# Kernel optimization log

Measured on AMD Instinct MI355X. Metric: run time of the kernel, lower is better.

The kernel has to match this reference:

```python
import jax, jax.numpy as jnp
import numpy as np

N = 50000   # nodes
E = 600000  # edges
D = 128     # in = hidden = out channels
L = 3       # num_layers
LN_EPS = 1e-5


def setup_inputs() -> dict:
    key = jax.random.key(0)
    ks = jax.random.split(key, 4)
    x = jax.random.normal(ks[0], (N, D), dtype=jnp.float32)
    edge_index = jax.random.randint(ks[1], (2, E), 0, N, dtype=jnp.int32)
    # GCNConv linear weights (glorot-ish scale) and biases, one per layer
    Ws = jax.random.normal(ks[2], (L, D, D), dtype=jnp.float32) / np.sqrt(D)
    bs = jnp.zeros((L, D), dtype=jnp.float32)
    # LayerNorm affine params per layer
    ln_w = jnp.ones((L, D), dtype=jnp.float32)
    ln_b = jnp.zeros((L, D), dtype=jnp.float32)
    # PReLU (single shared slope per layer, torch default init 0.25)
    alphas = jnp.full((L,), 0.25, dtype=jnp.float32)
    return {"x": x, "edge_index": edge_index, "Ws": Ws, "bs": bs,
            "ln_w": ln_w, "ln_b": ln_b, "alphas": alphas}


def reference(x, edge_index, Ws, bs, ln_w, ln_b, alphas):
    # --- gcn_norm: add self-loops, symmetric D^{-1/2} (A+I) D^{-1/2} ---
    loop = jnp.arange(N, dtype=edge_index.dtype)
    src = jnp.concatenate([edge_index[0], loop])  # [E+N]
    dst = jnp.concatenate([edge_index[1], loop])  # [E+N]
    deg = jax.ops.segment_sum(jnp.ones_like(dst, dtype=x.dtype), dst,
                              num_segments=N)
    dinv = jnp.where(deg > 0, jax.lax.rsqrt(jnp.maximum(deg, 1.0)), 0.0)
    norm = (dinv[src] * dinv[dst])[:, None]  # [E+N, 1]

    h = x
    for l in range(L):
        # GCNConv: linear -> gather -> scale -> scatter-add -> bias
        h = h @ Ws[l]                                   # [N, D]
        msg = h[src] * norm                             # [E+N, D]
        h = jax.ops.segment_sum(msg, dst, num_segments=N) + bs[l]
        # LayerNorm over feature dim
        mu = jnp.mean(h, axis=-1, keepdims=True)
        var = jnp.mean((h - mu) ** 2, axis=-1, keepdims=True)
        h = (h - mu) * jax.lax.rsqrt(var + LN_EPS) * ln_w[l] + ln_b[l]
        # PReLU
        h = jnp.where(h >= 0, h, alphas[l] * h)
    return h
```

## Files before the change

### kernel.cpp

```cpp
#include <hip/hip_runtime.h>
#include <hip/hip_bf16.h>

#define NN 50000
#define EE 600000
#define DD 128
#define LL 3
#define LN_EPS 1e-5f
#define CAP 64
#define ALD 136
#define POOL 16
#define NBLKS (NN / POOL)

typedef __attribute__((ext_vector_type(8))) short short8;
typedef __attribute__((ext_vector_type(4))) float floatx4;

__device__ inline unsigned short f2bf(float f) {
    union { float f; unsigned u; } a; a.f = f;
    unsigned r = a.u + 0x7fffu + ((a.u >> 16) & 1u);
    return (unsigned short)(r >> 16);
}


__global__ __launch_bounds__(256) void init_kernel(const float* __restrict__ W,
                                                   unsigned short* __restrict__ Wt,
                                                   int* __restrict__ cnt) {
    for (int i = blockIdx.x * 256 + threadIdx.x; i < NN; i += gridDim.x * 256)
        cnt[i] = 0;
    for (int i = blockIdx.x * 256 + threadIdx.x; i < LL * DD * DD; i += gridDim.x * 256) {
        int l = i >> 14, n = (i >> 7) & 127, k = i & 127;
        Wt[i] = f2bf(W[(l << 14) + k * DD + n]);
    }
}


__global__ __launch_bounds__(256) void gemm0_fill_kernel(
    const float* __restrict__ A, const unsigned short* __restrict__ Wt,
    const int* __restrict__ src, const int* __restrict__ dst,
    int* __restrict__ cnt, int* __restrict__ csrc,
    unsigned short* __restrict__ Cb) {
    __shared__ unsigned short alds[POOL * ALD];
    int tid = threadIdx.x;
    int lane = tid & 63;
    int w = tid >> 6;

    {
        int e = blockIdx.x * 256 + tid;
        if (e < EE) {
            int d = dst[e];
            int pos = atomicAdd(&cnt[d], 1);
            csrc[(size_t)d * CAP + pos] = src[e];
        }
    }

    {
        int row = tid >> 4;
        int kc = (tid & 15) * 8;
        const float* ap = &A[(size_t)(blockIdx.x * POOL + row) * DD + kc];
        float4 v0 = *(const float4*)&ap[0];
        float4 v1 = *(const float4*)&ap[4];
        float fv[8] = {v0.x, v0.y, v0.z, v0.w, v1.x, v1.y, v1.z, v1.w};
        unsigned short uv[8];
        #pragma unroll
        for (int q = 0; q < 8; q++) uv[q] = f2bf(fv[q]);
        *(uint4*)&alds[row * ALD + kc] = *(uint4*)&uv[0];
    }
    __syncthreads();

    int cbase = w * 32;
    int kq = (lane >> 4) * 8;
    int mrow = lane & 15;
    floatx4 acc[2] = {{0.f,0.f,0.f,0.f},{0.f,0.f,0.f,0.f}};
    #pragma unroll
    for (int t = 0; t < 4; t++) {
        short8 a = *(const short8*)&alds[mrow * ALD + t * 32 + kq];
        #pragma unroll
        for (int j = 0; j < 2; j++) {
            short8 b = *(const short8*)&Wt[(cbase + j * 16 + (lane & 15)) * DD + t * 32 + kq];
            acc[j] = __builtin_amdgcn_mfma_f32_16x16x32_bf16(a, b, acc[j], 0, 0, 0);
        }
    }
    __syncthreads();

    {
        int r0 = (lane >> 4) * 4;
        #pragma unroll
        for (int i = 0; i < 4; i++)
            #pragma unroll
            for (int j = 0; j < 2; j++)
                alds[(r0 + i) * ALD + cbase + j * 16 + (lane & 15)] = f2bf(acc[j][i]);
    }
    __syncthreads();
    {
        int srow = tid >> 4;
        int scol = (tid & 15) * 8;
        *(uint4*)&Cb[(size_t)(blockIdx.x * POOL + srow) * DD + scol] =
            *(uint4*)&alds[srow * ALD + scol];
    }
}


__device__ inline void acc_row_w(float* acc, uint4 t, float w) {
    unsigned uu[4] = {t.x, t.y, t.z, t.w};
    #pragma unroll
    for (int q = 0; q < 4; q++) {
        union { unsigned x; float f; } lo, hi;
        lo.x = uu[q] << 16;
        hi.x = uu[q] & 0xffff0000u;
        acc[2 * q]     += w * lo.f;
        acc[2 * q + 1] += w * hi.f;
    }
}

__device__ inline void agg_node(const unsigned short* __restrict__ Tb,
                                const int* __restrict__ cnt, const int* __restrict__ csrc,
                                const float* bv, const float* wv, const float* cv,
                                float alpha, int node, int f8, float* yv) {
    int deg = cnt[node];
    float dv = rsqrtf((float)(deg + 1));
    const int* row = &csrc[(size_t)node * CAP];

    float acc[8] = {};
    acc_row_w(acc, *(const uint4*)&Tb[(size_t)node * DD + f8], dv);

    int k = 0;
    for (; k + 4 <= deg; k += 4) {
        int4 ss = *(const int4*)&row[k];
        float w0 = rsqrtf((float)(cnt[ss.x] + 1));
        float w1 = rsqrtf((float)(cnt[ss.y] + 1));
        float w2 = rsqrtf((float)(cnt[ss.z] + 1));
        float w3 = rsqrtf((float)(cnt[ss.w] + 1));
        uint4 t0 = *(const uint4*)&Tb[(size_t)ss.x * DD + f8];
        uint4 t1 = *(const uint4*)&Tb[(size_t)ss.y * DD + f8];
        uint4 t2 = *(const uint4*)&Tb[(size_t)ss.z * DD + f8];
        uint4 t3 = *(const uint4*)&Tb[(size_t)ss.w * DD + f8];
        acc_row_w(acc, t0, w0); acc_row_w(acc, t1, w1);
        acc_row_w(acc, t2, w2); acc_row_w(acc, t3, w3);
    }
    for (; k < deg; k++) {
        int s = row[k];
        float w = rsqrtf((float)(cnt[s] + 1));
        acc_row_w(acc, *(const uint4*)&Tb[(size_t)s * DD + f8], w);
    }

    float a[8];
    float s1 = 0.f, s2 = 0.f;
    #pragma unroll
    for (int q = 0; q < 8; q++) {
        a[q] = fmaf(acc[q], dv, bv[q]);
        s1 += a[q]; s2 += a[q] * a[q];
    }
    #pragma unroll
    for (int off = 8; off > 0; off >>= 1) {
        s1 += __shfl_xor(s1, off, 16);
        s2 += __shfl_xor(s2, off, 16);
    }
    float mu = s1 * (1.f / DD);
    float var = s2 * (1.f / DD) - mu * mu;
    float rstd = rsqrtf(var + LN_EPS);
    #pragma unroll
    for (int q = 0; q < 8; q++) {
        float y = (a[q] - mu) * rstd * wv[q] + cv[q];
        yv[q] = (y >= 0.f) ? y : alpha * y;
    }
}


__global__ __launch_bounds__(256) void aggemm_kernel(
    const unsigned short* __restrict__ Tb, const int* __restrict__ cnt,
    const int* __restrict__ csrc,
    const float* __restrict__ bias, const float* __restrict__ lnw,
    const float* __restrict__ lnb, const float* __restrict__ alphas, int layer,
    const unsigned short* __restrict__ Wt, unsigned short* __restrict__ Tout) {
    __shared__ unsigned short alds[POOL * ALD];
    int tid = threadIdx.x;
    int g = tid >> 4;
    int lane16 = tid & 15;
    int f8 = lane16 * 8;
    int nodebase = blockIdx.x * POOL;

    float4 b0 = *(const float4*)&bias[f8];
    float4 b1 = *(const float4*)&bias[f8 + 4];
    float4 w0 = *(const float4*)&lnw[f8];
    float4 w1 = *(const float4*)&lnw[f8 + 4];
    float4 c0 = *(const float4*)&lnb[f8];
    float4 c1 = *(const float4*)&lnb[f8 + 4];
    float bv[8] = {b0.x, b0.y, b0.z, b0.w, b1.x, b1.y, b1.z, b1.w};
    float wv[8] = {w0.x, w0.y, w0.z, w0.w, w1.x, w1.y, w1.z, w1.w};
    float cv[8] = {c0.x, c0.y, c0.z, c0.w, c1.x, c1.y, c1.z, c1.w};
    float alpha = alphas[layer];

    {
        int node = nodebase + g;
        float yv[8];
        agg_node(Tb, cnt, csrc, bv, wv, cv, alpha, node, f8, yv);
        unsigned short pv[8];
        #pragma unroll
        for (int q = 0; q < 8; q++) pv[q] = f2bf(yv[q]);
        *(uint4*)&alds[g * ALD + f8] = *(uint4*)&pv[0];
    }
    __syncthreads();

    int lane = tid & 63;
    int w = tid >> 6;
    int cbase = w * 32;
    int kq = (lane >> 4) * 8;
    int mrow = lane & 15;
    floatx4 acc[2] = {{0.f,0.f,0.f,0.f},{0.f,0.f,0.f,0.f}};
    #pragma unroll
    for (int t = 0; t < 4; t++) {
        short8 a = *(const short8*)&alds[mrow * ALD + t * 32 + kq];
        #pragma unroll
        for (int j = 0; j < 2; j++) {
            short8 b = *(const short8*)&Wt[(cbase + j * 16 + (lane & 15)) * DD + t * 32 + kq];
            acc[j] = __builtin_amdgcn_mfma_f32_16x16x32_bf16(a, b, acc[j], 0, 0, 0);
        }
    }
    __syncthreads();

    {
        int r0 = (lane >> 4) * 4;
        #pragma unroll
        for (int i = 0; i < 4; i++)
            #pragma unroll
            for (int j = 0; j < 2; j++)
                alds[(r0 + i) * ALD + cbase + j * 16 + (lane & 15)] = f2bf(acc[j][i]);
    }
    __syncthreads();
    {
        int srow = tid >> 4;
        int scol = (tid & 15) * 8;
        *(uint4*)&Tout[(size_t)(nodebase + srow) * DD + scol] =
            *(uint4*)&alds[srow * ALD + scol];
    }
}


__global__ __launch_bounds__(256) void agg_final_kernel(
    const unsigned short* __restrict__ Tb, const int* __restrict__ cnt,
    const int* __restrict__ csrc,
    const float* __restrict__ bias, const float* __restrict__ lnw,
    const float* __restrict__ lnb, const float* __restrict__ alphas, int layer,
    float* __restrict__ out) {
    int g = threadIdx.x >> 4;
    int lane16 = threadIdx.x & 15;
    int f8 = lane16 * 8;
    int node = blockIdx.x * 16 + g;

    float4 b0 = *(const float4*)&bias[f8];
    float4 b1 = *(const float4*)&bias[f8 + 4];
    float4 w0 = *(const float4*)&lnw[f8];
    float4 w1 = *(const float4*)&lnw[f8 + 4];
    float4 c0 = *(const float4*)&lnb[f8];
    float4 c1 = *(const float4*)&lnb[f8 + 4];
    float bv[8] = {b0.x, b0.y, b0.z, b0.w, b1.x, b1.y, b1.z, b1.w};
    float wv[8] = {w0.x, w0.y, w0.z, w0.w, w1.x, w1.y, w1.z, w1.w};
    float cv[8] = {c0.x, c0.y, c0.z, c0.w, c1.x, c1.y, c1.z, c1.w};

    float yv[8];
    agg_node(Tb, cnt, csrc, bv, wv, cv, alphas[layer], node, f8, yv);

    float* op = &out[(size_t)node * DD + f8];
    *(float4*)&op[0] = make_float4(yv[0], yv[1], yv[2], yv[3]);
    *(float4*)&op[4] = make_float4(yv[4], yv[5], yv[6], yv[7]);
}


extern "C" void kernel_launch(void* const* d_in, const int* in_sizes, int n_in,
                              void* d_out, int out_size, void* d_ws, size_t ws_size,
                              hipStream_t stream) {
    const float* x    = (const float*)d_in[0];
    const int*   ei   = (const int*)d_in[1];
    const float* Ws   = (const float*)d_in[2];
    const float* bs   = (const float*)d_in[3];
    const float* lnw  = (const float*)d_in[4];
    const float* lnb  = (const float*)d_in[5];
    const float* alphas = (const float*)d_in[6];
    float* out = (float*)d_out;

    const int* src = ei;
    const int* dst = ei + EE;

    char* ws = (char*)d_ws;
    size_t off = 0;
    auto alloc = [&](size_t bytes) -> void* {
        void* p = ws + off;
        off = (off + bytes + 255) & ~(size_t)255;
        return p;
    };
    int* cnt  = (int*)alloc(NN * sizeof(int));
    int* csrc = (int*)alloc((size_t)NN * CAP * sizeof(int));
    unsigned short* wt    = (unsigned short*)alloc((size_t)LL * DD * DD * sizeof(unsigned short));
    unsigned short* tbufA = (unsigned short*)alloc((size_t)NN * DD * sizeof(unsigned short));
    unsigned short* tbufB = (unsigned short*)alloc((size_t)NN * DD * sizeof(unsigned short));

    init_kernel<<<256, 256, 0, stream>>>(Ws, wt, cnt);
    gemm0_fill_kernel<<<NBLKS, 256, 0, stream>>>(x, wt, src, dst, cnt, csrc, tbufA);

    aggemm_kernel<<<NBLKS, 256, 0, stream>>>(tbufA, cnt, csrc,
                                             bs + 0 * DD, lnw + 0 * DD, lnb + 0 * DD,
                                             alphas, 0, wt + 1 * DD * DD, tbufB);
    aggemm_kernel<<<NBLKS, 256, 0, stream>>>(tbufB, cnt, csrc,
                                             bs + 1 * DD, lnw + 1 * DD, lnb + 1 * DD,
                                             alphas, 1, wt + 2 * DD * DD, tbufA);
    agg_final_kernel<<<NBLKS, 256, 0, stream>>>(tbufA, cnt, csrc,
                                                bs + 2 * DD, lnw + 2 * DD, lnb + 2 * DD,
                                                alphas, 2, out);
}
```

Baseline: 233.2 us.

## Use persistent blocks with atomic ticket tile scheduling across all kernels

```diff
diff --git a/kernel.cpp b/kernel.cpp
--- a/kernel.cpp
+++ b/kernel.cpp
@@ -9,7 +9,8 @@
 #define CAP 64
 #define ALD 136
 #define POOL 16
-#define NBLKS (NN / POOL)
+#define NTILES (NN / POOL)
+#define GRID 2048
 
 typedef __attribute__((ext_vector_type(8))) short short8;
 typedef __attribute__((ext_vector_type(4))) float floatx4;
@@ -23,9 +24,11 @@
 
 __global__ __launch_bounds__(256) void init_kernel(const float* __restrict__ W,
                                                    unsigned short* __restrict__ Wt,
-                                                   int* __restrict__ cnt) {
+                                                   int* __restrict__ cnt,
+                                                   int* __restrict__ tk) {
     for (int i = blockIdx.x * 256 + threadIdx.x; i < NN; i += gridDim.x * 256)
         cnt[i] = 0;
+    if (blockIdx.x == 0 && threadIdx.x < 4) tk[threadIdx.x] = 0;
     for (int i = blockIdx.x * 256 + threadIdx.x; i < LL * DD * DD; i += gridDim.x * 256) {
         int l = i >> 14, n = (i >> 7) & 127, k = i & 127;
         Wt[i] = f2bf(W[(l << 14) + k * DD + n]);
@@ -37,64 +40,68 @@
     const float* __restrict__ A, const unsigned short* __restrict__ Wt,
     const int* __restrict__ src, const int* __restrict__ dst,
     int* __restrict__ cnt, int* __restrict__ csrc,
-    unsigned short* __restrict__ Cb) {
+    unsigned short* __restrict__ Cb, int* __restrict__ ticket) {
     __shared__ unsigned short alds[POOL * ALD];
+    __shared__ int s_t;
     int tid = threadIdx.x;
     int lane = tid & 63;
     int w = tid >> 6;
 
-    {
-        int e = blockIdx.x * 256 + tid;
-        if (e < EE) {
-            int d = dst[e];
-            int pos = atomicAdd(&cnt[d], 1);
-            csrc[(size_t)d * CAP + pos] = src[e];
-        }
-    }
-
-    {
-        int row = tid >> 4;
-        int kc = (tid & 15) * 8;
-        const float* ap = &A[(size_t)(blockIdx.x * POOL + row) * DD + kc];
-        float4 v0 = *(const float4*)&ap[0];
-        float4 v1 = *(const float4*)&ap[4];
-        float fv[8] = {v0.x, v0.y, v0.z, v0.w, v1.x, v1.y, v1.z, v1.w};
-        unsigned short uv[8];
-        #pragma unroll
-        for (int q = 0; q < 8; q++) uv[q] = f2bf(fv[q]);
-        *(uint4*)&alds[row * ALD + kc] = *(uint4*)&uv[0];
-    }
-    __syncthreads();
-
+    for (int e = blockIdx.x * 256 + tid; e < EE; e += GRID * 256) {
+        int d = dst[e];
+        int s = src[e];
+        int pos = atomicAdd(&cnt[d], 1);
+        csrc[(size_t)d * CAP + pos] = s;
+    }
+
+    int row = tid >> 4;
+    int kc = (tid & 15) * 8;
     int cbase = w * 32;
     int kq = (lane >> 4) * 8;
     int mrow = lane & 15;
-    floatx4 acc[2] = {{0.f,0.f,0.f,0.f},{0.f,0.f,0.f,0.f}};
-    #pragma unroll
-    for (int t = 0; t < 4; t++) {
-        short8 a = *(const short8*)&alds[mrow * ALD + t * 32 + kq];
+
+    for (;;) {
+        if (tid == 0) s_t = atomicAdd(ticket, 1);
+        __syncthreads();
+        int t = s_t;
+        if (t >= NTILES) break;
+        int nodebase = t * POOL;
+
+        {
+            const float* ap = &A[(size_t)(nodebase + row) * DD + kc];
+            float4 v0 = *(const float4*)&ap[0];
+            float4 v1 = *(const float4*)&ap[4];
+            float fv[8] = {v0.x, v0.y, v0.z, v0.w, v1.x, v1.y, v1.z, v1.w};
+            unsigned short uv[8];
+            #pragma unroll
+            for (int q = 0; q < 8; q++) uv[q] = f2bf(fv[q]);
+            *(uint4*)&alds[row * ALD + kc] = *(uint4*)&uv[0];
+        }
+        __syncthreads();
+
+        floatx4 acc[2] = {{0.f,0.f,0.f,0.f},{0.f,0.f,0.f,0.f}};
         #pragma unroll
-        for (int j = 0; j < 2; j++) {
-            short8 b = *(const short8*)&Wt[(cbase + j * 16 + (lane & 15)) * DD + t * 32 + kq];
-            acc[j] = __builtin_amdgcn_mfma_f32_16x16x32_bf16(a, b, acc[j], 0, 0, 0);
-        }
-    }
-    __syncthreads();
-
-    {
-        int r0 = (lane >> 4) * 4;
-        #pragma unroll
-        for (int i = 0; i < 4; i++)
-            #pragma unroll
-            for (int j = 0; j < 2; j++)
-                alds[(r0 + i) * ALD + cbase + j * 16 + (lane & 15)] = f2bf(acc[j][i]);
-    }
-    __syncthreads();
-    {
-        int srow = tid >> 4;
-        int scol = (tid & 15) * 8;
-        *(uint4*)&Cb[(size_t)(blockIdx.x * POOL + srow) * DD + scol] =
-            *(uint4*)&alds[srow * ALD + scol];
+        for (int t4 = 0; t4 < 4; t4++) {
+            short8 a = *(const short8*)&alds[mrow * ALD + t4 * 32 + kq];
+            #pragma unroll
+            for (int j = 0; j < 2; j++) {
+                short8 b = *(const short8*)&Wt[(cbase + j * 16 + (lane & 15)) * DD + t4 * 32 + kq];
+                acc[j] = __builtin_amdgcn_mfma_f32_16x16x32_bf16(a, b, acc[j], 0, 0, 0);
+            }
+        }
+        __syncthreads();
+
+        {
+            int r0 = (lane >> 4) * 4;
+            #pragma unroll
+            for (int i = 0; i < 4; i++)
+                #pragma unroll
+                for (int j = 0; j < 2; j++)
+                    alds[(r0 + i) * ALD + cbase + j * 16 + (lane & 15)] = f2bf(acc[j][i]);
+        }
+        __syncthreads();
+        *(uint4*)&Cb[(size_t)(nodebase + row) * DD + kc] =
+            *(uint4*)&alds[row * ALD + kc];
     }
 }
 
@@ -170,13 +177,14 @@
     const int* __restrict__ csrc,
     const float* __restrict__ bias, const float* __restrict__ lnw,
     const float* __restrict__ lnb, const float* __restrict__ alphas, int layer,
-    const unsigned short* __restrict__ Wt, unsigned short* __restrict__ Tout) {
+    const unsigned short* __restrict__ Wt, unsigned short* __restrict__ Tout,
+    int* __restrict__ ticket) {
     __shared__ unsigned short alds[POOL * ALD];
+    __shared__ int s_t;
     int tid = threadIdx.x;
     int g = tid >> 4;
     int lane16 = tid & 15;
     int f8 = lane16 * 8;
-    int nodebase = blockIdx.x * POOL;
 
     float4 b0 = *(const float4*)&bias[f8];
     float4 b1 = *(const float4*)&bias[f8 + 4];
@@ -189,48 +197,53 @@
     float cv[8] = {c0.x, c0.y, c0.z, c0.w, c1.x, c1.y, c1.z, c1.w};
     float alpha = alphas[layer];
 
-    {
-        int node = nodebase + g;
-        float yv[8];
-        agg_node(Tb, cnt, csrc, bv, wv, cv, alpha, node, f8, yv);
-        unsigned short pv[8];
-        #pragma unroll
-        for (int q = 0; q < 8; q++) pv[q] = f2bf(yv[q]);
-        *(uint4*)&alds[g * ALD + f8] = *(uint4*)&pv[0];
-    }
-    __syncthreads();
-
     int lane = tid & 63;
     int w = tid >> 6;
     int cbase = w * 32;
     int kq = (lane >> 4) * 8;
     int mrow = lane & 15;
-    floatx4 acc[2] = {{0.f,0.f,0.f,0.f},{0.f,0.f,0.f,0.f}};
-    #pragma unroll
-    for (int t = 0; t < 4; t++) {
-        short8 a = *(const short8*)&alds[mrow * ALD + t * 32 + kq];
+
+    for (;;) {
+        if (tid == 0) s_t = atomicAdd(ticket, 1);
+        __syncthreads();
+        int t = s_t;
+        if (t >= NTILES) break;
+        int nodebase = t * POOL;
+
+        {
+            int node = nodebase + g;
+            float yv[8];
+            agg_node(Tb, cnt, csrc, bv, wv, cv, alpha, node, f8, yv);
+            unsigned short pv[8];
+            #pragma unroll
+            for (int q = 0; q < 8; q++) pv[q] = f2bf(yv[q]);
+            *(uint4*)&alds[g * ALD + f8] = *(uint4*)&pv[0];
+        }
+        __syncthreads();
+
+        floatx4 acc[2] = {{0.f,0.f,0.f,0.f},{0.f,0.f,0.f,0.f}};
         #pragma unroll
-        for (int j = 0; j < 2; j++) {
-            short8 b = *(const short8*)&Wt[(cbase + j * 16 + (lane & 15)) * DD + t * 32 + kq];
-            acc[j] = __builtin_amdgcn_mfma_f32_16x16x32_bf16(a, b, acc[j], 0, 0, 0);
-        }
-    }
-    __syncthreads();
-
-    {
-        int r0 = (lane >> 4) * 4;
-        #pragma unroll
-        for (int i = 0; i < 4; i++)
-            #pragma unroll
-            for (int j = 0; j < 2; j++)
-                alds[(r0 + i) * ALD + cbase + j * 16 + (lane & 15)] = f2bf(acc[j][i]);
-    }
-    __syncthreads();
-    {
-        int srow = tid >> 4;
-        int scol = (tid & 15) * 8;
-        *(uint4*)&Tout[(size_t)(nodebase + srow) * DD + scol] =
-            *(uint4*)&alds[srow * ALD + scol];
+        for (int t4 = 0; t4 < 4; t4++) {
+            short8 a = *(const short8*)&alds[mrow * ALD + t4 * 32 + kq];
+            #pragma unroll
+            for (int j = 0; j < 2; j++) {
+                short8 b = *(const short8*)&Wt[(cbase + j * 16 + (lane & 15)) * DD + t4 * 32 + kq];
+                acc[j] = __builtin_amdgcn_mfma_f32_16x16x32_bf16(a, b, acc[j], 0, 0, 0);
+            }
+        }
+        __syncthreads();
+
+        {
+            int r0 = (lane >> 4) * 4;
+            #pragma unroll
+            for (int i = 0; i < 4; i++)
+                #pragma unroll
+                for (int j = 0; j < 2; j++)
+                    alds[(r0 + i) * ALD + cbase + j * 16 + (lane & 15)] = f2bf(acc[j][i]);
+        }
+        __syncthreads();
+        *(uint4*)&Tout[(size_t)(nodebase + g) * DD + f8] =
+            *(uint4*)&alds[g * ALD + f8];
     }
 }
 
@@ -240,11 +253,12 @@
     const int* __restrict__ csrc,
     const float* __restrict__ bias, const float* __restrict__ lnw,
     const float* __restrict__ lnb, const float* __restrict__ alphas, int layer,
-    float* __restrict__ out) {
-    int g = threadIdx.x >> 4;
-    int lane16 = threadIdx.x & 15;
+    float* __restrict__ out, int* __restrict__ ticket) {
+    __shared__ int s_t;
+    int tid = threadIdx.x;
+    int g = tid >> 4;
+    int lane16 = tid & 15;
     int f8 = lane16 * 8;
-    int node = blockIdx.x * 16 + g;
 
     float4 b0 = *(const float4*)&bias[f8];
     float4 b1 = *(const float4*)&bias[f8 + 4];
@@ -255,13 +269,22 @@
     float bv[8] = {b0.x, b0.y, b0.z, b0.w, b1.x, b1.y, b1.z, b1.w};
     float wv[8] = {w0.x, w0.y, w0.z, w0.w, w1.x, w1.y, w1.z, w1.w};
     float cv[8] = {c0.x, c0.y, c0.z, c0.w, c1.x, c1.y, c1.z, c1.w};
-
-    float yv[8];
-    agg_node(Tb, cnt, csrc, bv, wv, cv, alphas[layer], node, f8, yv);
-
-    float* op = &out[(size_t)node * DD + f8];
-    *(float4*)&op[0] = make_float4(yv[0], yv[1], yv[2], yv[3]);
-    *(float4*)&op[4] = make_float4(yv[4], yv[5], yv[6], yv[7]);
+    float alpha = alphas[layer];
+
+    for (;;) {
+        if (tid == 0) s_t = atomicAdd(ticket, 1);
+        __syncthreads();
+        int t = s_t;
+        if (t >= NTILES) break;
+        int node = t * POOL + g;
+
+        float yv[8];
+        agg_node(Tb, cnt, csrc, bv, wv, cv, alpha, node, f8, yv);
+
+        float* op = &out[(size_t)node * DD + f8];
+        *(float4*)&op[0] = make_float4(yv[0], yv[1], yv[2], yv[3]);
+        *(float4*)&op[4] = make_float4(yv[4], yv[5], yv[6], yv[7]);
+    }
 }
 
 
@@ -292,17 +315,18 @@
     unsigned short* wt    = (unsigned short*)alloc((size_t)LL * DD * DD * sizeof(unsigned short));
     unsigned short* tbufA = (unsigned short*)alloc((size_t)NN * DD * sizeof(unsigned short));
     unsigned short* tbufB = (unsigned short*)alloc((size_t)NN * DD * sizeof(unsigned short));
-
-    init_kernel<<<256, 256, 0, stream>>>(Ws, wt, cnt);
-    gemm0_fill_kernel<<<NBLKS, 256, 0, stream>>>(x, wt, src, dst, cnt, csrc, tbufA);
-
-    aggemm_kernel<<<NBLKS, 256, 0, stream>>>(tbufA, cnt, csrc,
-                                             bs + 0 * DD, lnw + 0 * DD, lnb + 0 * DD,
-                                             alphas, 0, wt + 1 * DD * DD, tbufB);
-    aggemm_kernel<<<NBLKS, 256, 0, stream>>>(tbufB, cnt, csrc,
-                                             bs + 1 * DD, lnw + 1 * DD, lnb + 1 * DD,
-                                             alphas, 1, wt + 2 * DD * DD, tbufA);
-    agg_final_kernel<<<NBLKS, 256, 0, stream>>>(tbufA, cnt, csrc,
-                                                bs + 2 * DD, lnw + 2 * DD, lnb + 2 * DD,
-                                                alphas, 2, out);
-}
+    int* tk = (int*)alloc(4 * sizeof(int));
+
+    init_kernel<<<256, 256, 0, stream>>>(Ws, wt, cnt, tk);
+    gemm0_fill_kernel<<<GRID, 256, 0, stream>>>(x, wt, src, dst, cnt, csrc, tbufA, tk + 0);
+
+    aggemm_kernel<<<GRID, 256, 0, stream>>>(tbufA, cnt, csrc,
+                                            bs + 0 * DD, lnw + 0 * DD, lnb + 0 * DD,
+                                            alphas, 0, wt + 1 * DD * DD, tbufB, tk + 1);
+    aggemm_kernel<<<GRID, 256, 0, stream>>>(tbufB, cnt, csrc,
+                                            bs + 1 * DD, lnw + 1 * DD, lnb + 1 * DD,
+                                            alphas, 1, wt + 2 * DD * DD, tbufA, tk + 2);
+    agg_final_kernel<<<GRID, 256, 0, stream>>>(tbufA, cnt, csrc,
+                                               bs + 2 * DD, lnw + 2 * DD, lnb + 2 * DD,
+                                               alphas, 2, out, tk + 3);
+}
```

Result: slower. 377.3 us (+61.8%).

## Prescale GEMM output by source dinv and split edge fill from first GEMM

Applied to the files above, without the earlier changes.

```diff
diff --git a/kernel.cpp b/kernel.cpp
--- a/kernel.cpp
+++ b/kernel.cpp
@@ -7,12 +7,15 @@
 #define LL 3
 #define LN_EPS 1e-5f
 #define CAP 64
+#define CNTS 16
 #define ALD 136
 #define POOL 16
-#define NBLKS (NN / POOL)
+#define NTILES (NN / POOL)
+#define FILLB ((EE + 255) / 256)
 
 typedef __attribute__((ext_vector_type(8))) short short8;
 typedef __attribute__((ext_vector_type(4))) float floatx4;
+typedef __attribute__((ext_vector_type(4))) unsigned uintx4;
 
 __device__ inline unsigned short f2bf(float f) {
     union { float f; unsigned u; } a; a.f = f;
@@ -20,42 +23,48 @@
     return (unsigned short)(r >> 16);
 }
 
-
-__global__ __launch_bounds__(256) void init_kernel(const float* __restrict__ W,
-                                                   unsigned short* __restrict__ Wt,
-                                                   int* __restrict__ cnt) {
-    for (int i = blockIdx.x * 256 + threadIdx.x; i < NN; i += gridDim.x * 256)
-        cnt[i] = 0;
-    for (int i = blockIdx.x * 256 + threadIdx.x; i < LL * DD * DD; i += gridDim.x * 256) {
+__device__ inline uintx4 gload4(const unsigned short* p) {
+    uintx4 r;
+    asm volatile("global_load_dwordx4 %0, %1, off" : "=v"(r) : "v"(p));
+    return r;
+}
+
+
+__global__ __launch_bounds__(256) void fill_kernel(
+    const float* __restrict__ W, unsigned short* __restrict__ Wt,
+    const int* __restrict__ src, const int* __restrict__ dst,
+    int* __restrict__ cnt, int* __restrict__ csrc) {
+    int e = blockIdx.x * 256 + threadIdx.x;
+    for (int i = e; i < LL * DD * DD; i += FILLB * 256) {
         int l = i >> 14, n = (i >> 7) & 127, k = i & 127;
         Wt[i] = f2bf(W[(l << 14) + k * DD + n]);
     }
-}
-
-
-__global__ __launch_bounds__(256) void gemm0_fill_kernel(
+    if (e < EE) {
+        int d = dst[e];
+        int s = src[e];
+        int pos = atomicAdd(&cnt[d * CNTS], 1);
+        csrc[(size_t)d * CAP + pos] = s;
+    }
+}
+
+
+__global__ __launch_bounds__(256) void gemm0_kernel(
     const float* __restrict__ A, const unsigned short* __restrict__ Wt,
-    const int* __restrict__ src, const int* __restrict__ dst,
-    int* __restrict__ cnt, int* __restrict__ csrc,
-    unsigned short* __restrict__ Cb) {
+    const int* __restrict__ cnt, unsigned short* __restrict__ Cb) {
     __shared__ unsigned short alds[POOL * ALD];
+    __shared__ float s_dinv[POOL];
     int tid = threadIdx.x;
     int lane = tid & 63;
     int w = tid >> 6;
-
-    {
-        int e = blockIdx.x * 256 + tid;
-        if (e < EE) {
-            int d = dst[e];
-            int pos = atomicAdd(&cnt[d], 1);
-            csrc[(size_t)d * CAP + pos] = src[e];
-        }
-    }
+    int nodebase = blockIdx.x * POOL;
+
+    if (tid < POOL)
+        s_dinv[tid] = rsqrtf((float)(cnt[(nodebase + tid) * CNTS] + 1));
 
     {
         int row = tid >> 4;
         int kc = (tid & 15) * 8;
-        const float* ap = &A[(size_t)(blockIdx.x * POOL + row) * DD + kc];
+        const float* ap = &A[(size_t)(nodebase + row) * DD + kc];
         float4 v0 = *(const float4*)&ap[0];
         float4 v1 = *(const float4*)&ap[4];
         float fv[8] = {v0.x, v0.y, v0.z, v0.w, v1.x, v1.y, v1.z, v1.w};
@@ -84,62 +93,65 @@
     {
         int r0 = (lane >> 4) * 4;
         #pragma unroll
-        for (int i = 0; i < 4; i++)
+        for (int i = 0; i < 4; i++) {
+            float dvr = s_dinv[r0 + i];
             #pragma unroll
             for (int j = 0; j < 2; j++)
-                alds[(r0 + i) * ALD + cbase + j * 16 + (lane & 15)] = f2bf(acc[j][i]);
+                alds[(r0 + i) * ALD + cbase + j * 16 + (lane & 15)] = f2bf(acc[j][i] * dvr);
+        }
     }
     __syncthreads();
     {
         int srow = tid >> 4;
         int scol = (tid & 15) * 8;
-        *(uint4*)&Cb[(size_t)(blockIdx.x * POOL + srow) * DD + scol] =
+        *(uint4*)&Cb[(size_t)(nodebase + srow) * DD + scol] =
             *(uint4*)&alds[srow * ALD + scol];
     }
 }
 
 
-__device__ inline void acc_row_w(float* acc, uint4 t, float w) {
-    unsigned uu[4] = {t.x, t.y, t.z, t.w};
+__device__ inline void acc_row(float* acc, uintx4 t) {
     #pragma unroll
     for (int q = 0; q < 4; q++) {
         union { unsigned x; float f; } lo, hi;
-        lo.x = uu[q] << 16;
-        hi.x = uu[q] & 0xffff0000u;
-        acc[2 * q]     += w * lo.f;
-        acc[2 * q + 1] += w * hi.f;
+        lo.x = t[q] << 16;
+        hi.x = t[q] & 0xffff0000u;
+        acc[2 * q]     += lo.f;
+        acc[2 * q + 1] += hi.f;
     }
 }
 
 __device__ inline void agg_node(const unsigned short* __restrict__ Tb,
                                 const int* __restrict__ cnt, const int* __restrict__ csrc,
                                 const float* bv, const float* wv, const float* cv,
-                                float alpha, int node, int f8, float* yv) {
-    int deg = cnt[node];
+                                float alpha, int node, int f8, float* yv, float* dv_out) {
+    int deg = cnt[node * CNTS];
     float dv = rsqrtf((float)(deg + 1));
+    *dv_out = dv;
     const int* row = &csrc[(size_t)node * CAP];
 
     float acc[8] = {};
-    acc_row_w(acc, *(const uint4*)&Tb[(size_t)node * DD + f8], dv);
+    acc_row(acc, *(const uintx4*)&Tb[((unsigned)node << 7) + f8]);
 
     int k = 0;
     for (; k + 4 <= deg; k += 4) {
         int4 ss = *(const int4*)&row[k];
-        float w0 = rsqrtf((float)(cnt[ss.x] + 1));
-        float w1 = rsqrtf((float)(cnt[ss.y] + 1));
-        float w2 = rsqrtf((float)(cnt[ss.z] + 1));
-        float w3 = rsqrtf((float)(cnt[ss.w] + 1));
-        uint4 t0 = *(const uint4*)&Tb[(size_t)ss.x * DD + f8];
-        uint4 t1 = *(const uint4*)&Tb[(size_t)ss.y * DD + f8];
-        uint4 t2 = *(const uint4*)&Tb[(size_t)ss.z * DD + f8];
-        uint4 t3 = *(const uint4*)&Tb[(size_t)ss.w * DD + f8];
-        acc_row_w(acc, t0, w0); acc_row_w(acc, t1, w1);
-        acc_row_w(acc, t2, w2); acc_row_w(acc, t3, w3);
+        const unsigned short* p0 = &Tb[((unsigned)ss.x << 7) + f8];
+        const unsigned short* p1 = &Tb[((unsigned)ss.y << 7) + f8];
+        const unsigned short* p2 = &Tb[((unsigned)ss.z << 7) + f8];
+        const unsigned short* p3 = &Tb[((unsigned)ss.w << 7) + f8];
+        uintx4 t0 = gload4(p0);
+        uintx4 t1 = gload4(p1);
+        uintx4 t2 = gload4(p2);
+        uintx4 t3 = gload4(p3);
+        asm volatile("s_waitcnt vmcnt(0)" ::: "memory");
+        __builtin_amdgcn_sched_barrier(0);
+        acc_row(acc, t0); acc_row(acc, t1);
+        acc_row(acc, t2); acc_row(acc, t3);
     }
     for (; k < deg; k++) {
         int s = row[k];
-        float w = rsqrtf((float)(cnt[s] + 1));
-        acc_row_w(acc, *(const uint4*)&Tb[(size_t)s * DD + f8], w);
+        acc_row(acc, *(const uintx4*)&Tb[((unsigned)s << 7) + f8]);
     }
 
     float a[8];
@@ -172,6 +184,7 @@
     const float* __restrict__ lnb, const float* __restrict__ alphas, int layer,
     const unsigned short* __restrict__ Wt, unsigned short* __restrict__ Tout) {
     __shared__ unsigned short alds[POOL * ALD];
+    __shared__ float s_dinv[POOL];
     int tid = threadIdx.x;
     int g = tid >> 4;
     int lane16 = tid & 15;
@@ -191,8 +204,9 @@
 
     {
         int node = nodebase + g;
-        float yv[8];
-        agg_node(Tb, cnt, csrc, bv, wv, cv, alpha, node, f8, yv);
+        float yv[8], dv;
+        agg_node(Tb, cnt, csrc, bv, wv, cv, alpha, node, f8, yv, &dv);
+        if (lane16 == 0) s_dinv[g] = dv;
         unsigned short pv[8];
         #pragma unroll
         for (int q = 0; q < 8; q++) pv[q] = f2bf(yv[q]);
@@ -220,10 +234,12 @@
     {
         int r0 = (lane >> 4) * 4;
         #pragma unroll
-        for (int i = 0; i < 4; i++)
+        for (int i = 0; i < 4; i++) {
+            float dvr = s_dinv[r0 + i];
             #pragma unroll
             for (int j = 0; j < 2; j++)
-                alds[(r0 + i) * ALD + cbase + j * 16 + (lane & 15)] = f2bf(acc[j][i]);
+                alds[(r0 + i) * ALD + cbase + j * 16 + (lane & 15)] = f2bf(acc[j][i] * dvr);
+        }
     }
     __syncthreads();
     {
@@ -244,7 +260,7 @@
     int g = threadIdx.x >> 4;
     int lane16 = threadIdx.x & 15;
     int f8 = lane16 * 8;
-    int node = blockIdx.x * 16 + g;
+    int node = blockIdx.x * POOL + g;
 
     float4 b0 = *(const float4*)&bias[f8];
     float4 b1 = *(const float4*)&bias[f8 + 4];
@@ -256,8 +272,8 @@
     float wv[8] = {w0.x, w0.y, w0.z, w0.w, w1.x, w1.y, w1.z, w1.w};
     float cv[8] = {c0.x, c0.y, c0.z, c0.w, c1.x, c1.y, c1.z, c1.w};
 
-    float yv[8];
-    agg_node(Tb, cnt, csrc, bv, wv, cv, alphas[layer], node, f8, yv);
+    float yv[8], dv;
+    agg_node(Tb, cnt, csrc, bv, wv, cv, alphas[layer], node, f8, yv, &dv);
 
     float* op = &out[(size_t)node * DD + f8];
     *(float4*)&op[0] = make_float4(yv[0], yv[1], yv[2], yv[3]);
@@ -287,22 +303,23 @@
         off = (off + bytes + 255) & ~(size_t)255;
         return p;
     };
-    int* cnt  = (int*)alloc(NN * sizeof(int));
+    int* cnt  = (int*)alloc((size_t)NN * CNTS * sizeof(int));
     int* csrc = (int*)alloc((size_t)NN * CAP * sizeof(int));
     unsigned short* wt    = (unsigned short*)alloc((size_t)LL * DD * DD * sizeof(unsigned short));
     unsigned short* tbufA = (unsigned short*)alloc((size_t)NN * DD * sizeof(unsigned short));
     unsigned short* tbufB = (unsigned short*)alloc((size_t)NN * DD * sizeof(unsigned short));
 
-    init_kernel<<<256, 256, 0, stream>>>(Ws, wt, cnt);
-    gemm0_fill_kernel<<<NBLKS, 256, 0, stream>>>(x, wt, src, dst, cnt, csrc, tbufA);
-
-    aggemm_kernel<<<NBLKS, 256, 0, stream>>>(tbufA, cnt, csrc,
-                                             bs + 0 * DD, lnw + 0 * DD, lnb + 0 * DD,
-                                             alphas, 0, wt + 1 * DD * DD, tbufB);
-    aggemm_kernel<<<NBLKS, 256, 0, stream>>>(tbufB, cnt, csrc,
-                                             bs + 1 * DD, lnw + 1 * DD, lnb + 1 * DD,
-                                             alphas, 1, wt + 2 * DD * DD, tbufA);
-    agg_final_kernel<<<NBLKS, 256, 0, stream>>>(tbufA, cnt, csrc,
-                                                bs + 2 * DD, lnw + 2 * DD, lnb + 2 * DD,
-                                                alphas, 2, out);
-}
+    hipMemsetAsync(cnt, 0, (size_t)NN * CNTS * sizeof(int), stream);
+    fill_kernel<<<FILLB, 256, 0, stream>>>(Ws, wt, src, dst, cnt, csrc);
+    gemm0_kernel<<<NTILES, 256, 0, stream>>>(x, wt, cnt, tbufA);
+
+    aggemm_kernel<<<NTILES, 256, 0, stream>>>(tbufA, cnt, csrc,
+                                              bs + 0 * DD, lnw + 0 * DD, lnb + 0 * DD,
+                                              alphas, 0, wt + 1 * DD * DD, tbufB);
+    aggemm_kernel<<<NTILES, 256, 0, stream>>>(tbufB, cnt, csrc,
+                                              bs + 1 * DD, lnw + 1 * DD, lnb + 1 * DD,
+                                              alphas, 1, wt + 2 * DD * DD, tbufA);
+    agg_final_kernel<<<NTILES, 256, 0, stream>>>(tbufA, cnt, csrc,
+                                                 bs + 2 * DD, lnw + 2 * DD, lnb + 2 * DD,
+                                                 alphas, 2, out);
+}
```

Measured after the change: 233.2 us. About the same (-0.0%).
